# Optimization experiments

Hardware: AMD Instinct MI355X
Metric: run time of the kernel (lower is better)

Reference implementation:

```python
import jax, jax.numpy as jnp
import numpy as np

NUM_HEADS = 12

def setup_inputs() -> dict:
    key = jax.random.key(0)
    ks = jax.random.split(key, 6)
    B, Nq, Nkv, C = 2, 2048, 2048, 768
    q_token = jax.random.normal(ks[0], (B, Nq, C), dtype=jnp.float32)
    kv_token = jax.random.normal(ks[1], (B, Nkv, C), dtype=jnp.float32)
    s = 1.0 / np.sqrt(C)
    Wq = jax.random.normal(ks[2], (C, C), dtype=jnp.float32) * s
    Wkv = jax.random.normal(ks[3], (C, 2 * C), dtype=jnp.float32) * s
    Wproj = jax.random.normal(ks[4], (C, C), dtype=jnp.float32) * s
    bproj = jnp.zeros((C,), dtype=jnp.float32)
    return {"q_token": q_token, "kv_token": kv_token, "Wq": Wq, "Wkv": Wkv, "Wproj": Wproj, "bproj": bproj}

def reference(q_token, kv_token, Wq, Wkv, Wproj, bproj):
    B, Nq, C = q_token.shape
    H = NUM_HEADS
    D = C // H
    scale = D ** -0.5
    # Q: [B, H, Nq, D]
    Q = (q_token @ Wq).reshape(B, Nq, H, D).transpose(0, 2, 1, 3)
    # KV: token layout is (2, H, D) on last dim -> [2, B, H, Nkv, D]
    Nkv = kv_token.shape[1]
    KV = (kv_token @ Wkv).reshape(B, Nkv, 2, H, D).transpose(2, 0, 3, 1, 4)
    K, V = KV[0], KV[1]
    attn = jnp.einsum('bhqd,bhkd->bhqk', Q, K) * scale
    attn = jax.nn.softmax(attn, axis=-1)
    # NOTE: original code multiplies by scale again here (faithful quirk)
    x = jnp.einsum('bhqk,bhkd->bhqd', attn, V) * scale
    x = x.transpose(0, 2, 1, 3).reshape(B, Nq, C)
    return x @ Wproj + bproj
```

## Files before the change

### kernel.cpp

```cpp
#include <hip/hip_runtime.h>

typedef __attribute__((ext_vector_type(8))) short short8;
typedef __attribute__((ext_vector_type(4))) float f32x4;
typedef __attribute__((ext_vector_type(16))) float f32x16;
typedef __attribute__((ext_vector_type(4))) unsigned u32x4;

__device__ __forceinline__ unsigned short f2bf(float f) {
  unsigned u = __builtin_bit_cast(unsigned, f);
  u += 0x7fffu + ((u >> 16) & 1u);
  return (unsigned short)(u >> 16);
}

__device__ __forceinline__ unsigned cvt_pk_bf16(float a, float b) {
  unsigned r;
  asm("v_cvt_pk_bf16_f32 %0, %1, %2" : "=v"(r) : "v"(a), "v"(b));
  return r;
}

__device__ __forceinline__ void gload_lds16(const unsigned short* g, unsigned short* l) {
  __builtin_amdgcn_global_load_lds((const __attribute__((address_space(1))) unsigned int*)g,
                                   (__attribute__((address_space(3))) unsigned int*)l, 16, 0, 0);
}

__global__ __launch_bounds__(256) void cvt_tr(
    const float* __restrict__ q_token, const float* __restrict__ kv_token,
    const float* __restrict__ Wq, const float* __restrict__ Wkv, const float* __restrict__ Wp,
    unsigned short* __restrict__ qb, unsigned short* __restrict__ kvb,
    unsigned short* __restrict__ wqT, unsigned short* __restrict__ wkvT,
    unsigned short* __restrict__ wpT) {
  __shared__ float tile[32][33];
  const int tid = threadIdx.x;
  int bx = blockIdx.x;
  if (bx < 6144) {
    int i = bx * 256 + tid;
    const float* in = (i < 786432) ? q_token : kv_token;
    unsigned short* out = (i < 786432) ? qb : kvb;
    int j = (i < 786432) ? i : i - 786432;
    float4 v = ((const float4*)in)[j];
    ushort4 o;
    o.x = f2bf(v.x); o.y = f2bf(v.y); o.z = f2bf(v.z); o.w = f2bf(v.w);
    ((ushort4*)out)[j] = o;
    return;
  }
  bx -= 6144;
  int gx = bx % 96, gy = bx / 96;
  const float* in; unsigned short* out; int C;
  if (gx < 24)       { in = Wq;  out = wqT;  C = 768;  }
  else if (gx < 72)  { in = Wkv; out = wkvT; C = 1536; gx -= 24; }
  else               { in = Wp;  out = wpT;  C = 768;  gx -= 72; }
  const int R = 768;
  int c0 = gx * 32, r0 = gy * 32;
  int tx = tid & 31, ty = tid >> 5;
  for (int i = ty; i < 32; i += 8)
    tile[i][tx] = in[(size_t)(r0 + i) * C + c0 + tx];
  __syncthreads();
  for (int i = ty; i < 32; i += 8)
    out[(size_t)(c0 + i) * R + r0 + tx] = f2bf(tile[tx][i]);
}

__global__ __launch_bounds__(256) void gemm_qkv(
    const unsigned short* __restrict__ Aq, const unsigned short* __restrict__ Akv,
    const unsigned short* __restrict__ BtQ, const unsigned short* __restrict__ BtKV,
    unsigned short* __restrict__ Qo, unsigned short* __restrict__ Ko,
    unsigned short* __restrict__ Vo) {
  __shared__ __align__(16) unsigned short A_lds[128][64];
  __shared__ __align__(16) unsigned short B_lds[128][64];
  const bool isQ = blockIdx.y < 6;
  const unsigned short* A  = isQ ? Aq : Akv;
  const unsigned short* Bt = isQ ? BtQ : BtKV;
  const int yy = isQ ? blockIdx.y : blockIdx.y - 6;
  const int K = 768;
  const int tile_m = blockIdx.x * 128;
  const int tile_n = yy * 128;
  const int tid = threadIdx.x;
  const int wid = tid >> 6, lane = tid & 63;
  const int wm = (wid >> 1) * 64, wn = (wid & 1) * 64;
  const int lr = lane & 15, lg = lane >> 4;
  const int s_row = (lane >> 3);
  const int s_col = (lane & 7) * 8;
  f32x4 acc[4][4] = {};

  for (int k0 = 0; k0 < K; k0 += 64) {
    __syncthreads();
#pragma unroll
    for (int j = 0; j < 4; ++j) {
      const int c = wid * 4 + j;
      const int row = c * 8 + s_row;
      gload_lds16(&A[(size_t)(tile_m + row) * K + k0 + s_col], &A_lds[0][0] + c * 512);
      gload_lds16(&Bt[(size_t)(tile_n + row) * K + k0 + s_col], &B_lds[0][0] + c * 512);
    }
    __syncthreads();
    short8 a[4][2], b[4][2];
#pragma unroll
    for (int i = 0; i < 4; ++i)
#pragma unroll
      for (int t = 0; t < 2; ++t) {
        a[i][t] = *(const short8*)&A_lds[wm + i * 16 + lr][t * 32 + lg * 8];
        b[i][t] = *(const short8*)&B_lds[wn + i * 16 + lr][t * 32 + lg * 8];
      }
#pragma unroll
    for (int i = 0; i < 4; ++i)
#pragma unroll
      for (int j = 0; j < 4; ++j)
#pragma unroll
        for (int t = 0; t < 2; ++t)
          acc[i][j] = __builtin_amdgcn_mfma_f32_16x16x32_bf16(a[i][t], b[j][t], acc[i][j], 0, 0, 0);
  }

#pragma unroll
  for (int i = 0; i < 4; ++i)
#pragma unroll
    for (int j = 0; j < 4; ++j)
#pragma unroll
      for (int r = 0; r < 4; ++r) {
        int m = tile_m + wm + i * 16 + lg * 4 + r;
        int n = tile_n + wn + j * 16 + lr;
        float v = acc[i][j][r];
        int b = m >> 11, row = m & 2047;
        if (isQ) {
          int h = n >> 6, d = n & 63;
          Qo[((size_t)((b * 12 + h) * 2048 + row) << 6) + d] = f2bf(v);
        } else {
          if (n < 768) {
            int h = n >> 6, d = n & 63;
            Ko[((size_t)((b * 12 + h) * 2048 + row) << 6) + d] = f2bf(v);
          } else {
            int h = (n - 768) >> 6, d = n & 63;
            Vo[((size_t)((b * 12 + h) * 64 + d) << 11) + row] = f2bf(v);
          }
        }
      }
}

__global__ __launch_bounds__(256) void gemm_proj(
    const unsigned short* __restrict__ A, const unsigned short* __restrict__ Bt,
    float* __restrict__ outf, const float* __restrict__ bias) {
  __shared__ __align__(16) unsigned short A_lds[64][64];
  __shared__ __align__(16) unsigned short B_lds[64][64];
  const int K = 768, N = 768;
  const int tile_m = blockIdx.x * 64;
  const int tile_n = blockIdx.y * 64;
  const int tid = threadIdx.x;
  const int wid = tid >> 6, lane = tid & 63;
  const int wm = (wid >> 1) * 32, wn = (wid & 1) * 32;
  const int lr = lane & 15, lg = lane >> 4;
  const int s_r8 = lane >> 3;
  const int s_col = (lane & 7) * 8;
  f32x4 acc[2][2] = {};

  for (int k0 = 0; k0 < K; k0 += 64) {
    __syncthreads();
#pragma unroll
    for (int i = 0; i < 2; ++i) {
      const int row = (wid * 2 + i) * 8 + s_r8;
      gload_lds16(&A[(size_t)(tile_m + row) * K + k0 + s_col], &A_lds[0][0] + (wid * 2 + i) * 512);
      gload_lds16(&Bt[(size_t)(tile_n + row) * K + k0 + s_col], &B_lds[0][0] + (wid * 2 + i) * 512);
    }
    __syncthreads();
    short8 a[2][2], b[2][2];
#pragma unroll
    for (int i = 0; i < 2; ++i)
#pragma unroll
      for (int t = 0; t < 2; ++t) {
        a[i][t] = *(const short8*)&A_lds[wm + i * 16 + lr][t * 32 + lg * 8];
        b[i][t] = *(const short8*)&B_lds[wn + i * 16 + lr][t * 32 + lg * 8];
      }
#pragma unroll
    for (int i = 0; i < 2; ++i)
#pragma unroll
      for (int j = 0; j < 2; ++j)
#pragma unroll
        for (int t = 0; t < 2; ++t)
          acc[i][j] = __builtin_amdgcn_mfma_f32_16x16x32_bf16(a[i][t], b[j][t], acc[i][j], 0, 0, 0);
  }

#pragma unroll
  for (int i = 0; i < 2; ++i)
#pragma unroll
    for (int j = 0; j < 2; ++j)
#pragma unroll
      for (int r = 0; r < 4; ++r) {
        int m = tile_m + wm + i * 16 + lg * 4 + r;
        int n = tile_n + wn + j * 16 + lr;
        outf[(size_t)m * N + n] = acc[i][j][r] + bias[n];
      }
}

__global__ __launch_bounds__(256, 3) void attn_fwd(
    const unsigned short* __restrict__ Q, const unsigned short* __restrict__ Kb,
    const unsigned short* __restrict__ Vt, unsigned short* __restrict__ X) {
  __shared__ __align__(16) unsigned short SMEM[16384];
  __shared__ float m_lds[4][32];
  __shared__ float l_lds[4][64];
  const int bid = blockIdx.x;
  const int bh = bid % 24;
  const int q0 = (bid / 24) * 64;
  const int tid = threadIdx.x, wid = tid >> 6, lane = tid & 63;
  const int l31 = lane & 31, hi = lane >> 5;
  const int grp = wid >> 1;
  const int qsub = wid & 1;
  const float Cc = 0.18033688011112042f;
  const float THRS = 44.3614195558365f;

  const unsigned short* Kbase = Kb + (size_t)bh * (2048 * 64);
  const unsigned short* Vbase = Vt + (size_t)bh * (64 * 2048);

  short8 qf[4];
  {
    const unsigned short* Qp = Q + ((size_t)bh * 2048 + q0 + qsub * 32 + l31) * 64 + hi * 8;
#pragma unroll
    for (int t = 0; t < 4; ++t) qf[t] = *(const short8*)&Qp[t * 16];
  }

  f32x16 accO0 = {}, accO1 = {};
  float m_run = -1e30f, l_run = 0.f;

  const int gtid = tid & 127;
  const int s_row = gtid >> 3;
  const int s_chk = gtid & 7;
  unsigned short* Kst0 = SMEM + grp * 8192;
  unsigned short* Kst1 = SMEM + grp * 8192 + 4096;
  const int fr = l31 & 7;

  {
    const int kvb = grp * 1024;
#pragma unroll
    for (int p = 0; p < 4; ++p) {
      const int row = p * 16 + s_row;
      float4 v = *(const float4*)&Kbase[(size_t)(kvb + row) * 64 + s_chk * 8];
      *(float4*)&Kst0[row * 64 + ((s_chk ^ (row & 7)) << 3)] = v;
    }
  }
  __syncthreads();

  for (int t = 0; t < 16; ++t) {
    const int cur = t & 1;
    const int kv0 = grp * 1024 + t * 64;
    float4 nK[4];
    if (t < 15) {
#pragma unroll
      for (int p = 0; p < 4; ++p) {
        const int row = p * 16 + s_row;
        nK[p] = *(const float4*)&Kbase[(size_t)(kv0 + 64 + row) * 64 + s_chk * 8];
      }
    }
    short8 vf[8];
#pragma unroll
    for (int s = 0; s < 4; ++s) {
      vf[s]     = *(const short8*)&Vbase[(size_t)l31 * 2048 + kv0 + s * 16 + hi * 8];
      vf[4 + s] = *(const short8*)&Vbase[(size_t)(32 + l31) * 2048 + kv0 + s * 16 + hi * 8];
    }
    const unsigned short* KL = cur ? Kst1 : Kst0;
    f32x16 S0 = {}, S1 = {};
    __builtin_amdgcn_s_setprio(1);
#pragma unroll
    for (int t4 = 0; t4 < 4; ++t4) {
      const int ca = ((2 * t4 + hi) ^ fr) << 3;
      short8 k0 = *(const short8*)&KL[l31 * 64 + ca];
      short8 k1 = *(const short8*)&KL[(32 + l31) * 64 + ca];
      S0 = __builtin_amdgcn_mfma_f32_32x32x16_bf16(k0, qf[t4], S0, 0, 0, 0);
      S1 = __builtin_amdgcn_mfma_f32_32x32x16_bf16(k1, qf[t4], S1, 0, 0, 0);
    }
    __builtin_amdgcn_s_setprio(0);
    float mx[8];
#pragma unroll
    for (int g = 0; g < 4; ++g) {
      mx[g]     = fmaxf(fmaxf(S0[4 * g], S0[4 * g + 1]), fmaxf(S0[4 * g + 2], S0[4 * g + 3]));
      mx[4 + g] = fmaxf(fmaxf(S1[4 * g], S1[4 * g + 1]), fmaxf(S1[4 * g + 2], S1[4 * g + 3]));
    }
    float rmax = fmaxf(fmaxf(fmaxf(mx[0], mx[1]), fmaxf(mx[2], mx[3])),
                       fmaxf(fmaxf(mx[4], mx[5]), fmaxf(mx[6], mx[7])));
    rmax = fmaxf(rmax, __shfl_xor(rmax, 32));
    if (!__all(rmax <= m_run + THRS)) {
      float mnew = fmaxf(m_run, rmax);
      float alpha = exp2f((m_run - mnew) * Cc);
      m_run = mnew;
      l_run *= alpha;
#pragma unroll
      for (int r = 0; r < 16; ++r) { accO0[r] *= alpha; accO1[r] *= alpha; }
    }
    const float mC = m_run * Cc;
#pragma unroll
    for (int r = 0; r < 16; ++r) {
      S0[r] = exp2f(fmaf(S0[r], Cc, -mC));
      S1[r] = exp2f(fmaf(S1[r], Cc, -mC));
    }
    float ts[8];
#pragma unroll
    for (int g = 0; g < 4; ++g) {
      ts[g]     = (S0[4 * g] + S0[4 * g + 1]) + (S0[4 * g + 2] + S0[4 * g + 3]);
      ts[4 + g] = (S1[4 * g] + S1[4 * g + 1]) + (S1[4 * g + 2] + S1[4 * g + 3]);
    }
    l_run += ((ts[0] + ts[1]) + (ts[2] + ts[3])) + ((ts[4] + ts[5]) + (ts[6] + ts[7]));
    unsigned w0[8], w1[8];
#pragma unroll
    for (int j = 0; j < 4; ++j) {
      w0[j]     = cvt_pk_bf16(S0[4 * j],     S0[4 * j + 1]);
      w1[j]     = cvt_pk_bf16(S0[4 * j + 2], S0[4 * j + 3]);
      w0[4 + j] = cvt_pk_bf16(S1[4 * j],     S1[4 * j + 1]);
      w1[4 + j] = cvt_pk_bf16(S1[4 * j + 2], S1[4 * j + 3]);
    }
    __builtin_amdgcn_s_setprio(1);
#pragma unroll
    for (int s = 0; s < 4; ++s) {
      unsigned A0 = w0[2 * s], B0 = w0[2 * s + 1];
      unsigned A1 = w1[2 * s], B1 = w1[2 * s + 1];
      unsigned A0s = (unsigned)__shfl_xor((int)A0, 32);
      unsigned B0s = (unsigned)__shfl_xor((int)B0, 32);
      unsigned A1s = (unsigned)__shfl_xor((int)A1, 32);
      unsigned B1s = (unsigned)__shfl_xor((int)B1, 32);
      unsigned X0 = hi ? B0s : A0;
      unsigned X1 = hi ? B1s : A1;
      unsigned X2 = hi ? B0 : A0s;
      unsigned X3 = hi ? B1 : A1s;
      u32x4 pw = {X0, X1, X2, X3};
      short8 pfrag = __builtin_bit_cast(short8, pw);
      accO0 = __builtin_amdgcn_mfma_f32_32x32x16_bf16(vf[s], pfrag, accO0, 0, 0, 0);
      accO1 = __builtin_amdgcn_mfma_f32_32x32x16_bf16(vf[4 + s], pfrag, accO1, 0, 0, 0);
    }
    __builtin_amdgcn_s_setprio(0);
    if (t < 15) {
      unsigned short* KN = cur ? Kst0 : Kst1;
#pragma unroll
      for (int p = 0; p < 4; ++p) {
        const int row = p * 16 + s_row;
        *(float4*)&KN[row * 64 + ((s_chk ^ (row & 7)) << 3)] = nK[p];
      }
    }
    __syncthreads();
  }

  float* Ob = (float*)SMEM;
#pragma unroll
  for (int dt = 0; dt < 2; ++dt) {
    const f32x16& acc = dt ? accO1 : accO0;
#pragma unroll
    for (int r = 0; r < 16; ++r)
      Ob[wid * 2048 + (dt * 16 + r) * 64 + hi * 32 + l31] = acc[r];
  }
  if (hi == 0) m_lds[wid][l31] = m_run;
  l_lds[wid][hi * 32 + l31] = l_run;
  __syncthreads();

  {
    const int qs = wid >> 1, dh = wid & 1;
    const int sl0 = qs, sl1 = qs + 2;
    float m0 = m_lds[sl0][l31], m1 = m_lds[sl1][l31];
    float M = fmaxf(m0, m1);
    float w0s = exp2f((m0 - M) * Cc);
    float w1s = exp2f((m1 - M) * Cc);
    float ltot = w0s * (l_lds[sl0][l31] + l_lds[sl0][32 + l31])
               + w1s * (l_lds[sl1][l31] + l_lds[sl1][32 + l31]);
    const float inv = 0.125f / ltot;
    const int b = bh / 12, h = bh % 12;
    short8 os0, os1;
#pragma unroll
    for (int j = 0; j < 16; ++j) {
      const int d = dh * 32 + hi * 16 + j;
      const int dt = d >> 5, crow = d & 31;
      const int hs = (crow >> 2) & 1;
      const int rr = (crow & 3) | ((crow >> 3) << 2);
      float v = w0s * Ob[sl0 * 2048 + (dt * 16 + rr) * 64 + hs * 32 + l31]
              + w1s * Ob[sl1 * 2048 + (dt * 16 + rr) * 64 + hs * 32 + l31];
      if (j < 8) os0[j] = (short)f2bf(v * inv);
      else       os1[j - 8] = (short)f2bf(v * inv);
    }
    const int q = q0 + qs * 32 + l31;
    unsigned short* Xp = X + ((size_t)b * 2048 + q) * 768 + h * 64 + dh * 32 + hi * 16;
    *(short8*)Xp = os0;
    *(short8*)(Xp + 8) = os1;
  }
}

extern "C" void kernel_launch(void* const* d_in, const int* in_sizes, int n_in,
                              void* d_out, int out_size, void* d_ws, size_t ws_size,
                              hipStream_t stream) {
  const float* q_token  = (const float*)d_in[0];
  const float* kv_token = (const float*)d_in[1];
  const float* Wq    = (const float*)d_in[2];
  const float* Wkv   = (const float*)d_in[3];
  const float* Wproj = (const float*)d_in[4];
  const float* bproj = (const float*)d_in[5];
  float* out = (float*)d_out;

  unsigned short* qb   = (unsigned short*)d_ws;
  unsigned short* kvb  = qb   + 3145728;
  unsigned short* wqT  = kvb  + 3145728;
  unsigned short* wkvT = wqT  + 589824;
  unsigned short* wpT  = wkvT + 1179648;
  unsigned short* Qb   = wpT  + 589824;
  unsigned short* Kbf  = Qb   + 3145728;
  unsigned short* Vtb  = Kbf  + 3145728;
  unsigned short* Xb   = Vtb  + 3145728;

  cvt_tr<<<8448, 256, 0, stream>>>(q_token, kv_token, Wq, Wkv, Wproj,
                                   qb, kvb, wqT, wkvT, wpT);

  gemm_qkv<<<dim3(32, 18), 256, 0, stream>>>(qb, kvb, wqT, wkvT, Qb, Kbf, Vtb);

  attn_fwd<<<768, 256, 0, stream>>>(Qb, Kbf, Vtb, Xb);

  gemm_proj<<<dim3(64, 12), 256, 0, stream>>>(Xb, wpT, out, bproj);
}
```

Before: 132.1 us.

## Triple-buffer K tiles via direct global-to-LDS loads with prefetch depth two

Replaces the register-staged double-buffered K loads with global_load_lds DMA into a three-slot LDS ring, issuing loads two tiles ahead and waiting with explicit vmcnt counters before a raw s_barrier. This removes the register round-trip and the LDS store instructions and gives loads more time to land behind compute. It raises LDS use per block from 32KB to 48KB, which may limit the three-blocks-per-CU occupancy target. It also relies on careful vmcnt accounting, since V loads are also in flight.

New measurement: 135.8 us. 2.8% more time.

```diff
diff --git a/kernel.cpp b/kernel.cpp
--- a/kernel.cpp
+++ b/kernel.cpp
@@ -189,7 +189,7 @@
 __global__ __launch_bounds__(256, 3) void attn_fwd(
     const unsigned short* __restrict__ Q, const unsigned short* __restrict__ Kb,
     const unsigned short* __restrict__ Vt, unsigned short* __restrict__ X) {
-  __shared__ __align__(16) unsigned short SMEM[16384];
+  __shared__ __align__(16) unsigned short SMEM[24576];
   __shared__ float m_lds[4][32];
   __shared__ float l_lds[4][64];
   const int bid = blockIdx.x;
@@ -199,6 +199,7 @@
   const int l31 = lane & 31, hi = lane >> 5;
   const int grp = wid >> 1;
   const int qsub = wid & 1;
+  const int gw = wid & 1;
   const float Cc = 0.18033688011112042f;
   const float THRS = 44.3614195558365f;
 
@@ -215,42 +216,38 @@
   f32x16 accO0 = {}, accO1 = {};
   float m_run = -1e30f, l_run = 0.f;
 
-  const int gtid = tid & 127;
-  const int s_row = gtid >> 3;
-  const int s_chk = gtid & 7;
-  unsigned short* Kst0 = SMEM + grp * 8192;
-  unsigned short* Kst1 = SMEM + grp * 8192 + 4096;
+  const int r8 = lane >> 3;
+  const int scc = ((lane & 7) ^ r8) << 3;
+  unsigned short* Kgrp = SMEM + grp * 12288;
   const int fr = l31 & 7;
 
-  {
-    const int kvb = grp * 1024;
-#pragma unroll
-    for (int p = 0; p < 4; ++p) {
-      const int row = p * 16 + s_row;
-      float4 v = *(const float4*)&Kbase[(size_t)(kvb + row) * 64 + s_chk * 8];
-      *(float4*)&Kst0[row * 64 + ((s_chk ^ (row & 7)) << 3)] = v;
-    }
-  }
-  __syncthreads();
-
+#define STAGE_K(BUF, TT)                                                               \
+  {                                                                                    \
+    const int kvs_ = grp * 1024 + (TT) * 64;                                           \
+    unsigned short* db_ = Kgrp + (BUF) * 4096 + gw * 512;                              \
+    _Pragma("unroll")                                                                  \
+    for (int i2 = 0; i2 < 4; ++i2)                                                     \
+      gload_lds16(&Kbase[(size_t)(kvs_ + i2 * 16 + gw * 8 + r8) * 64 + scc],           \
+                  db_ + i2 * 1024);                                                    \
+  }
+
+  STAGE_K(0, 0)
+  STAGE_K(1, 1)
+  __builtin_amdgcn_sched_barrier(0);
+  asm volatile("s_waitcnt vmcnt(4)" ::: "memory");
+  __builtin_amdgcn_sched_barrier(0);
+  __builtin_amdgcn_s_barrier();
+
+  int bufc = 0;
   for (int t = 0; t < 16; ++t) {
-    const int cur = t & 1;
     const int kv0 = grp * 1024 + t * 64;
-    float4 nK[4];
-    if (t < 15) {
-#pragma unroll
-      for (int p = 0; p < 4; ++p) {
-        const int row = p * 16 + s_row;
-        nK[p] = *(const float4*)&Kbase[(size_t)(kv0 + 64 + row) * 64 + s_chk * 8];
-      }
-    }
     short8 vf[8];
 #pragma unroll
     for (int s = 0; s < 4; ++s) {
       vf[s]     = *(const short8*)&Vbase[(size_t)l31 * 2048 + kv0 + s * 16 + hi * 8];
       vf[4 + s] = *(const short8*)&Vbase[(size_t)(32 + l31) * 2048 + kv0 + s * 16 + hi * 8];
     }
-    const unsigned short* KL = cur ? Kst1 : Kst0;
+    const unsigned short* KL = Kgrp + bufc * 4096;
     f32x16 S0 = {}, S1 = {};
     __builtin_amdgcn_s_setprio(1);
 #pragma unroll
@@ -319,16 +316,20 @@
       accO1 = __builtin_amdgcn_mfma_f32_32x32x16_bf16(vf[4 + s], pfrag, accO1, 0, 0, 0);
     }
     __builtin_amdgcn_s_setprio(0);
-    if (t < 15) {
-      unsigned short* KN = cur ? Kst0 : Kst1;
-#pragma unroll
-      for (int p = 0; p < 4; ++p) {
-        const int row = p * 16 + s_row;
-        *(float4*)&KN[row * 64 + ((s_chk ^ (row & 7)) << 3)] = nK[p];
-      }
-    }
-    __syncthreads();
-  }
+    __builtin_amdgcn_sched_barrier(0);
+    if (t < 14) {
+      int bufn = bufc + 2; if (bufn >= 3) bufn -= 3;
+      STAGE_K(bufn, t + 2)
+      __builtin_amdgcn_sched_barrier(0);
+      asm volatile("s_waitcnt vmcnt(4)" ::: "memory");
+    } else {
+      asm volatile("s_waitcnt vmcnt(0)" ::: "memory");
+    }
+    __builtin_amdgcn_sched_barrier(0);
+    __builtin_amdgcn_s_barrier();
+    bufc += 1; if (bufc >= 3) bufc -= 3;
+  }
+#undef STAGE_K
 
   float* Ob = (float*)SMEM;
 #pragma unroll
```
